# Kernel optimization log

Hardware: AMD Instinct MI355X
Metric: run time of the kernel (lower is better)

Reference implementation:

```python
import jax, jax.numpy as jnp
import numpy as np

N = 50000      # nodes
E = 800000     # edges (avg degree 16)
DN = 128       # in_node_feats (== out_feats)
DE = 64        # in_edge_feats
DO = 128       # out_feats


def setup_inputs() -> dict:
    key = jax.random.key(0)
    k1, k2, k3, k4, k5 = jax.random.split(key, 5)
    node_feats = jax.random.normal(k1, (N, DN), dtype=jnp.float32)
    edge_feats = jax.random.normal(k2, (E, DE), dtype=jnp.float32)
    src = jax.random.randint(k3, (E,), 0, N, dtype=jnp.int64) if jax.config.jax_enable_x64 else jax.random.randint(k3, (E,), 0, N).astype(jnp.int32)
    dst = jax.random.randint(k4, (E,), 0, N).astype(src.dtype)
    # nn.Linear(2*DN+DE, DO): weight [DO, 2*DN+DE], bias [DO]
    W = jax.random.normal(k5, (DO, 2 * DN + DE), dtype=jnp.float32) * 0.05
    b = jnp.zeros((DO,), dtype=jnp.float32)
    return {"node_feats": node_feats, "edge_feats": edge_feats, "W": W, "b": b, "src": src, "dst": dst}


def reference(node_feats, edge_feats, W, b, src, dst):
    # message: linear(cat([h_src, h_dst, e_f])) per edge -> [E, DO]
    msg_in = jnp.concatenate([node_feats[src], node_feats[dst], edge_feats], axis=1)  # [E, 2*DN+DE]
    mail = msg_in @ W.T + b                                                           # [E, DO]
    # scatter-mean at destination nodes (DGL mailbox mean)
    sums = jax.ops.segment_sum(mail, dst, num_segments=N)                             # [N, DO]
    deg = jax.ops.segment_sum(jnp.ones((mail.shape[0],), mail.dtype), dst, num_segments=N)  # [N]
    mean = sums / jnp.maximum(deg, 1.0)[:, None]
    # nodes with no incoming messages keep their original h (DGL update_all semantics)
    h = jnp.where(deg[:, None] > 0, mean, node_feats)
    # activation (relu); dropout is identity in eval / p=0
    return jax.nn.relu(h)
```

## Files before the change

### kernel.cpp

```cpp
#include <hip/hip_runtime.h>

#define DN 128
#define DE 64
#define DO 128
#define DIN 320
#define LDX 72
#define PAD 64

typedef short bf16x8 __attribute__((ext_vector_type(8)));
typedef float f32x4 __attribute__((ext_vector_type(4)));
typedef unsigned long long u64;

__device__ inline unsigned short f2bf(float f) {
    unsigned u = __builtin_bit_cast(unsigned, f);
    u = (u + 0x7fffu + ((u >> 16) & 1u)) >> 16;
    return (unsigned short)u;
}
__device__ inline unsigned pk2(float a, float b) {
    return (unsigned)f2bf(a) | ((unsigned)f2bf(b) << 16);
}
__device__ inline float bf2f(unsigned short h) {
    unsigned u = ((unsigned)h) << 16;
    return __builtin_bit_cast(float, u);
}
__device__ inline unsigned f2fp8(float f) {
    unsigned u = __builtin_bit_cast(unsigned, f * 0x1p-120f);
    unsigned s = (u >> 24) & 0x80u;
    u &= 0x7fffffffu;
    unsigned r = (u + 0x7ffffu + ((u >> 20) & 1u)) >> 20;
    if (r > 0x7eu) r = 0x7eu;
    return s | r;
}
__device__ inline float fp8_acc(unsigned b, float acc) {
    unsigned u = ((b & 0x80u) << 24) | ((b & 0x7fu) << 20);
    return fmaf(__builtin_bit_cast(float, u), 0x1p120f, acc);
}

__global__ __launch_bounds__(256) void convert_kernel(
    const float* __restrict__ W, const float* __restrict__ nf,
    unsigned short* __restrict__ Wbf, unsigned short* __restrict__ nfbf,
    unsigned char* __restrict__ nf8, int* __restrict__ cursor,
    int nW4, int n4tot, int N)
{
    int i = blockIdx.x * 256 + threadIdx.x;
    if (i < N) cursor[i] = 0;
    if (i >= n4tot) return;
    if (i < nW4) {
        const float4 v = *(const float4*)&W[(size_t)i * 4];
        u64 val = (u64)pk2(v.x, v.y) | ((u64)pk2(v.z, v.w) << 32);
        *(u64*)&Wbf[(size_t)i * 4] = val;
    } else {
        int j = i - nW4;
        const float4 v = *(const float4*)&nf[(size_t)j * 4];
        u64 val = (u64)pk2(v.x, v.y) | ((u64)pk2(v.z, v.w) << 32);
        *(u64*)&nfbf[(size_t)j * 4] = val;
        unsigned p8 = f2fp8(v.x) | (f2fp8(v.y) << 8) |
                      (f2fp8(v.z) << 16) | (f2fp8(v.w) << 24);
        *(unsigned*)&nf8[(size_t)j * 4] = p8;
    }
}

__global__ __launch_bounds__(256) void fill_kernel(
    const int* __restrict__ dst, const int* __restrict__ src,
    int* __restrict__ cursor, u64* __restrict__ es, int E)
{
    int e = blockIdx.x * 256 + threadIdx.x;
    if (e >= E) return;
    int d = dst[e];
    int s = src[e];
    int pos = atomicAdd(&cursor[d], 1);
    if (pos < PAD)
        es[(size_t)d * PAD + pos] = (u64)(unsigned)e | ((u64)(unsigned)s << 32);
}

__global__ __launch_bounds__(256) void gather_kernel(
    const unsigned char* __restrict__ nf8, const float* __restrict__ ef,
    const u64* __restrict__ es, const int* __restrict__ cursor,
    unsigned short* __restrict__ agg_src_bf,
    unsigned short* __restrict__ agg_edge_bf, int N)
{
    const int wave = threadIdx.x >> 6;
    const int lane = threadIdx.x & 63;
    const int v = blockIdx.x * 4 + wave;
    if (v >= N) return;

    const int cnt = min(cursor[v], PAD);

    const int g = lane >> 4;
    const int q = lane & 15;

    float accN[8];
#pragma unroll
    for (int j = 0; j < 8; ++j) accN[j] = 0.f;
    f32x4 accE = {0.f, 0.f, 0.f, 0.f};

    int e_l = 0, s_l = 0;
    if (lane < cnt) {
        u64 p = __builtin_nontemporal_load(&es[(size_t)v * PAD + lane]);
        e_l = (int)(unsigned)(p & 0xffffffffu);
        s_l = (int)(unsigned)(p >> 32);
    }
    for (int i = 0; i < cnt; i += 16) {
        const int s0 = __shfl(s_l, i + g, 64);
        const int s1 = __shfl(s_l, i + 4 + g, 64);
        const int s2 = __shfl(s_l, i + 8 + g, 64);
        const int s3 = __shfl(s_l, i + 12 + g, 64);
        const int e0 = __shfl(e_l, i + g, 64);
        const int e1 = __shfl(e_l, i + 4 + g, 64);
        const int e2 = __shfl(e_l, i + 8 + g, 64);
        const int e3 = __shfl(e_l, i + 12 + g, 64);
        u64 n0 = *(const u64*)&nf8[(size_t)s0 * DN + q * 8];
        u64 n1 = *(const u64*)&nf8[(size_t)s1 * DN + q * 8];
        u64 n2 = *(const u64*)&nf8[(size_t)s2 * DN + q * 8];
        u64 n3 = *(const u64*)&nf8[(size_t)s3 * DN + q * 8];
        f32x4 f0 = __builtin_nontemporal_load((const f32x4*)&ef[(size_t)e0 * DE + q * 4]);
        f32x4 f1 = __builtin_nontemporal_load((const f32x4*)&ef[(size_t)e1 * DE + q * 4]);
        f32x4 f2 = __builtin_nontemporal_load((const f32x4*)&ef[(size_t)e2 * DE + q * 4]);
        f32x4 f3 = __builtin_nontemporal_load((const f32x4*)&ef[(size_t)e3 * DE + q * 4]);
        if (i + g < cnt) {
#pragma unroll
            for (int j = 0; j < 8; ++j) accN[j] = fp8_acc((unsigned)(n0 >> (j * 8)) & 0xffu, accN[j]);
            accE += f0;
        }
        if (i + 4 + g < cnt) {
#pragma unroll
            for (int j = 0; j < 8; ++j) accN[j] = fp8_acc((unsigned)(n1 >> (j * 8)) & 0xffu, accN[j]);
            accE += f1;
        }
        if (i + 8 + g < cnt) {
#pragma unroll
            for (int j = 0; j < 8; ++j) accN[j] = fp8_acc((unsigned)(n2 >> (j * 8)) & 0xffu, accN[j]);
            accE += f2;
        }
        if (i + 12 + g < cnt) {
#pragma unroll
            for (int j = 0; j < 8; ++j) accN[j] = fp8_acc((unsigned)(n3 >> (j * 8)) & 0xffu, accN[j]);
            accE += f3;
        }
    }

#pragma unroll
    for (int j = 0; j < 8; ++j) {
        accN[j] += __shfl_xor(accN[j], 16, 64);
        accN[j] += __shfl_xor(accN[j], 32, 64);
    }
#pragma unroll
    for (int j = 0; j < 4; ++j) {
        accE[j] += __shfl_xor(accE[j], 16, 64);
        accE[j] += __shfl_xor(accE[j], 32, 64);
    }

    const float inv = (cnt > 0) ? (1.0f / (float)cnt) : 0.0f;
    if (g == 0) {
        uint4 val;
        val.x = pk2(accN[0] * inv, accN[1] * inv);
        val.y = pk2(accN[2] * inv, accN[3] * inv);
        val.z = pk2(accN[4] * inv, accN[5] * inv);
        val.w = pk2(accN[6] * inv, accN[7] * inv);
        *(uint4*)&agg_src_bf[(size_t)v * DN + q * 8] = val;
    } else if (g == 1) {
        u64 val = (u64)pk2(accE[0] * inv, accE[1] * inv) |
                  ((u64)pk2(accE[2] * inv, accE[3] * inv) << 32);
        *(u64*)&agg_edge_bf[(size_t)v * DE + q * 4] = val;
    }
}

__global__ __launch_bounds__(256) void finalize_kernel(
    const float* __restrict__ nf, const unsigned short* __restrict__ nfbf,
    const unsigned short* __restrict__ Wbf, const float* __restrict__ b,
    const unsigned short* __restrict__ agg_src_bf,
    const unsigned short* __restrict__ agg_edge_bf,
    const int* __restrict__ cursor, float* __restrict__ out, int N)
{
    __shared__ unsigned short Ws[DO * LDX];
    __shared__ unsigned short Xs[64 * LDX];
    __shared__ float bs[DO];
    __shared__ int degs[64];

    const int tid = threadIdx.x;
    const int lane = tid & 63;
    const int w = tid >> 6;
    const int node0 = blockIdx.x * 64;

    if (tid < DO) bs[tid] = b[tid];
    if (tid < 64) {
        int v = node0 + tid;
        degs[tid] = (v < N) ? cursor[v] : 0;
    }

    f32x4 acc[8];
#pragma unroll
    for (int r = 0; r < 8; ++r) acc[r] = (f32x4){0.f, 0.f, 0.f, 0.f};

    for (int c = 0; c < 5; ++c) {
        const int k0 = c * 64;
        __syncthreads();
#pragma unroll
        for (int it = 0; it < 8; ++it) {
            int i4 = tid + it * 256;
            int o = i4 >> 4;
            int kk = (i4 & 15) * 4;
            *(u64*)&Ws[o * LDX + kk] = *(const u64*)&Wbf[o * DIN + k0 + kk];
        }
#pragma unroll
        for (int it = 0; it < 4; ++it) {
            int i4 = tid + it * 256;
            int n = i4 >> 4;
            int kk = (i4 & 15) * 4;
            int v = node0 + n;
            u64 val = 0;
            if (v < N) {
                if (c < 2) {
                    val = *(const u64*)&agg_src_bf[(size_t)v * DN + k0 + kk];
                } else if (c < 4) {
                    val = *(const u64*)&nfbf[(size_t)v * DN + (c - 2) * 64 + kk];
                } else {
                    val = *(const u64*)&agg_edge_bf[(size_t)v * DE + kk];
                }
            }
            *(u64*)&Xs[n * LDX + kk] = val;
        }
        __syncthreads();

        const int xrow = 16 * w + (lane & 15);
        const int kgrp = (lane >> 4) * 8;
#pragma unroll
        for (int t = 0; t < 2; ++t) {
            bf16x8 a = *(const bf16x8*)&Xs[xrow * LDX + t * 32 + kgrp];
#pragma unroll
            for (int r = 0; r < 8; ++r) {
                bf16x8 bw = *(const bf16x8*)&Ws[(16 * r + (lane & 15)) * LDX + t * 32 + kgrp];
                acc[r] = __builtin_amdgcn_mfma_f32_16x16x32_bf16(a, bw, acc[r], 0, 0, 0);
            }
        }
    }

    const int col = lane & 15;
#pragma unroll
    for (int r = 0; r < 8; ++r) {
        const int o = 16 * r + col;
        const float bo = bs[o];
#pragma unroll
        for (int reg = 0; reg < 4; ++reg) {
            const int n = 16 * w + (lane >> 4) * 4 + reg;
            const int v = node0 + n;
            if (v >= N) continue;
            float val = (degs[n] > 0) ? (acc[r][reg] + bo) : nf[(size_t)v * DN + o];
            __builtin_nontemporal_store(fmaxf(val, 0.0f), &out[(size_t)v * DO + o]);
        }
    }
}

extern "C" void kernel_launch(void* const* d_in, const int* in_sizes, int n_in,
                              void* d_out, int out_size, void* d_ws, size_t ws_size,
                              hipStream_t stream)
{
    const float* nf  = (const float*)d_in[0];
    const float* ef  = (const float*)d_in[1];
    const float* W   = (const float*)d_in[2];
    const float* b   = (const float*)d_in[3];
    const int*   src = (const int*)d_in[4];
    const int*   dst = (const int*)d_in[5];
    float* out = (float*)d_out;

    const int N = in_sizes[0] / DN;
    const int E = in_sizes[4];

    char* p = (char*)d_ws;
    int* cursor = (int*)p;  p += (size_t)N * 4;
    p = (char*)(((uintptr_t)p + 15) & ~(uintptr_t)15);
    u64* es     = (u64*)p;  p += (size_t)N * PAD * 8;
    unsigned short* agg_src_bf  = (unsigned short*)p;  p += (size_t)N * DN * 2;
    unsigned short* agg_edge_bf = (unsigned short*)p;  p += (size_t)N * DE * 2;
    unsigned short* nfbf        = (unsigned short*)p;  p += (size_t)N * DN * 2;
    unsigned char*  nf8         = (unsigned char*)p;   p += (size_t)N * DN;
    unsigned short* Wbf         = (unsigned short*)p;

    const int nW4 = DO * DIN / 4;
    const int n4tot = nW4 + N * DN / 4;
    convert_kernel<<<(n4tot + 255) / 256, 256, 0, stream>>>(
        W, nf, Wbf, nfbf, nf8, cursor, nW4, n4tot, N);

    const int eb = (E + 255) / 256;
    fill_kernel<<<eb, 256, 0, stream>>>(dst, src, cursor, es, E);

    const int gb = (N + 3) / 4;
    gather_kernel<<<gb, 256, 0, stream>>>(nf8, ef, es, cursor,
                                          agg_src_bf, agg_edge_bf, N);

    const int nb = (N + 63) / 64;
    finalize_kernel<<<nb, 256, 0, stream>>>(nf, nfbf, Wbf, b, agg_src_bf,
                                            agg_edge_bf, cursor, out, N);
}
```

Before: 133.7 us.

## Merge convert and fill kernels; gather two nodes per wave

The dtype conversion and the CSR bucket fill now run in one kernel over a combined index range, and the cursor is zeroed with a memset instead of inside the convert kernel. This trades one kernel launch for a memset. The gather kernel now handles two destination nodes per wave, issuing twice as many independent loads per iteration to hide memory latency. The cost is more registers, which can lower occupancy, and iterating to the larger of the two degrees.

Result: slower. 167.1 us (+25.0%).

```diff
diff --git a/kernel.cpp b/kernel.cpp
--- a/kernel.cpp
+++ b/kernel.cpp
@@ -18,10 +18,6 @@
 }
 __device__ inline unsigned pk2(float a, float b) {
     return (unsigned)f2bf(a) | ((unsigned)f2bf(b) << 16);
-}
-__device__ inline float bf2f(unsigned short h) {
-    unsigned u = ((unsigned)h) << 16;
-    return __builtin_bit_cast(float, u);
 }
 __device__ inline unsigned f2fp8(float f) {
     unsigned u = __builtin_bit_cast(unsigned, f * 0x1p-120f);
@@ -36,41 +32,39 @@
     return fmaf(__builtin_bit_cast(float, u), 0x1p120f, acc);
 }
 
-__global__ __launch_bounds__(256) void convert_kernel(
+__global__ __launch_bounds__(256) void prep_kernel(
     const float* __restrict__ W, const float* __restrict__ nf,
     unsigned short* __restrict__ Wbf, unsigned short* __restrict__ nfbf,
-    unsigned char* __restrict__ nf8, int* __restrict__ cursor,
-    int nW4, int n4tot, int N)
+    unsigned char* __restrict__ nf8,
+    const int* __restrict__ dst, const int* __restrict__ src,
+    int* __restrict__ cursor, u64* __restrict__ es,
+    int nW4, int n4tot, int E)
 {
-    int i = blockIdx.x * 256 + threadIdx.x;
-    if (i < N) cursor[i] = 0;
-    if (i >= n4tot) return;
-    if (i < nW4) {
-        const float4 v = *(const float4*)&W[(size_t)i * 4];
-        u64 val = (u64)pk2(v.x, v.y) | ((u64)pk2(v.z, v.w) << 32);
-        *(u64*)&Wbf[(size_t)i * 4] = val;
+    int gid = blockIdx.x * 256 + threadIdx.x;
+    if (gid < n4tot) {
+        if (gid < nW4) {
+            const float4 v = *(const float4*)&W[(size_t)gid * 4];
+            u64 val = (u64)pk2(v.x, v.y) | ((u64)pk2(v.z, v.w) << 32);
+            *(u64*)&Wbf[(size_t)gid * 4] = val;
+        } else {
+            int j = gid - nW4;
+            const float4 v = *(const float4*)&nf[(size_t)j * 4];
+            u64 val = (u64)pk2(v.x, v.y) | ((u64)pk2(v.z, v.w) << 32);
+            *(u64*)&nfbf[(size_t)j * 4] = val;
+            unsigned p8 = f2fp8(v.x) | (f2fp8(v.y) << 8) |
+                          (f2fp8(v.z) << 16) | (f2fp8(v.w) << 24);
+            *(unsigned*)&nf8[(size_t)j * 4] = p8;
+        }
     } else {
-        int j = i - nW4;
-        const float4 v = *(const float4*)&nf[(size_t)j * 4];
-        u64 val = (u64)pk2(v.x, v.y) | ((u64)pk2(v.z, v.w) << 32);
-        *(u64*)&nfbf[(size_t)j * 4] = val;
-        unsigned p8 = f2fp8(v.x) | (f2fp8(v.y) << 8) |
-                      (f2fp8(v.z) << 16) | (f2fp8(v.w) << 24);
-        *(unsigned*)&nf8[(size_t)j * 4] = p8;
-    }
-}
-
-__global__ __launch_bounds__(256) void fill_kernel(
-    const int* __restrict__ dst, const int* __restrict__ src,
-    int* __restrict__ cursor, u64* __restrict__ es, int E)
-{
-    int e = blockIdx.x * 256 + threadIdx.x;
-    if (e >= E) return;
-    int d = dst[e];
-    int s = src[e];
-    int pos = atomicAdd(&cursor[d], 1);
-    if (pos < PAD)
-        es[(size_t)d * PAD + pos] = (u64)(unsigned)e | ((u64)(unsigned)s << 32);
+        int e = gid - n4tot;
+        if (e < E) {
+            int d = dst[e];
+            int s = src[e];
+            int pos = atomicAdd(&cursor[d], 1);
+            if (pos < PAD)
+                es[(size_t)d * PAD + pos] = (u64)(unsigned)e | ((u64)(unsigned)s << 32);
+        }
+    }
 }
 
 __global__ __launch_bounds__(256) void gather_kernel(
@@ -81,87 +75,150 @@
 {
     const int wave = threadIdx.x >> 6;
     const int lane = threadIdx.x & 63;
-    const int v = blockIdx.x * 4 + wave;
-    if (v >= N) return;
-
-    const int cnt = min(cursor[v], PAD);
+    const int v0 = blockIdx.x * 8 + wave * 2;
+    const int v1 = v0 + 1;
+    if (v0 >= N) return;
 
     const int g = lane >> 4;
     const int q = lane & 15;
 
-    float accN[8];
-#pragma unroll
-    for (int j = 0; j < 8; ++j) accN[j] = 0.f;
-    f32x4 accE = {0.f, 0.f, 0.f, 0.f};
-
-    int e_l = 0, s_l = 0;
-    if (lane < cnt) {
-        u64 p = __builtin_nontemporal_load(&es[(size_t)v * PAD + lane]);
-        e_l = (int)(unsigned)(p & 0xffffffffu);
-        s_l = (int)(unsigned)(p >> 32);
-    }
-    for (int i = 0; i < cnt; i += 16) {
-        const int s0 = __shfl(s_l, i + g, 64);
-        const int s1 = __shfl(s_l, i + 4 + g, 64);
-        const int s2 = __shfl(s_l, i + 8 + g, 64);
-        const int s3 = __shfl(s_l, i + 12 + g, 64);
-        const int e0 = __shfl(e_l, i + g, 64);
-        const int e1 = __shfl(e_l, i + 4 + g, 64);
-        const int e2 = __shfl(e_l, i + 8 + g, 64);
-        const int e3 = __shfl(e_l, i + 12 + g, 64);
-        u64 n0 = *(const u64*)&nf8[(size_t)s0 * DN + q * 8];
-        u64 n1 = *(const u64*)&nf8[(size_t)s1 * DN + q * 8];
-        u64 n2 = *(const u64*)&nf8[(size_t)s2 * DN + q * 8];
-        u64 n3 = *(const u64*)&nf8[(size_t)s3 * DN + q * 8];
-        f32x4 f0 = __builtin_nontemporal_load((const f32x4*)&ef[(size_t)e0 * DE + q * 4]);
-        f32x4 f1 = __builtin_nontemporal_load((const f32x4*)&ef[(size_t)e1 * DE + q * 4]);
-        f32x4 f2 = __builtin_nontemporal_load((const f32x4*)&ef[(size_t)e2 * DE + q * 4]);
-        f32x4 f3 = __builtin_nontemporal_load((const f32x4*)&ef[(size_t)e3 * DE + q * 4]);
-        if (i + g < cnt) {
-#pragma unroll
-            for (int j = 0; j < 8; ++j) accN[j] = fp8_acc((unsigned)(n0 >> (j * 8)) & 0xffu, accN[j]);
-            accE += f0;
-        }
-        if (i + 4 + g < cnt) {
-#pragma unroll
-            for (int j = 0; j < 8; ++j) accN[j] = fp8_acc((unsigned)(n1 >> (j * 8)) & 0xffu, accN[j]);
-            accE += f1;
-        }
-        if (i + 8 + g < cnt) {
-#pragma unroll
-            for (int j = 0; j < 8; ++j) accN[j] = fp8_acc((unsigned)(n2 >> (j * 8)) & 0xffu, accN[j]);
-            accE += f2;
-        }
-        if (i + 12 + g < cnt) {
-#pragma unroll
-            for (int j = 0; j < 8; ++j) accN[j] = fp8_acc((unsigned)(n3 >> (j * 8)) & 0xffu, accN[j]);
-            accE += f3;
+    const int cnt0 = min(cursor[v0], PAD);
+    const int cnt1 = (v1 < N) ? min(cursor[v1], PAD) : 0;
+
+    float accNA[8], accNB[8];
+#pragma unroll
+    for (int j = 0; j < 8; ++j) { accNA[j] = 0.f; accNB[j] = 0.f; }
+    f32x4 accEA = {0.f, 0.f, 0.f, 0.f};
+    f32x4 accEB = {0.f, 0.f, 0.f, 0.f};
+
+    int eA = 0, sA = 0, eB = 0, sB = 0;
+    if (lane < cnt0) {
+        u64 p = __builtin_nontemporal_load(&es[(size_t)v0 * PAD + lane]);
+        eA = (int)(unsigned)(p & 0xffffffffu);
+        sA = (int)(unsigned)(p >> 32);
+    }
+    if (lane < cnt1) {
+        u64 p = __builtin_nontemporal_load(&es[(size_t)v1 * PAD + lane]);
+        eB = (int)(unsigned)(p & 0xffffffffu);
+        sB = (int)(unsigned)(p >> 32);
+    }
+
+    const int cmax = max(cnt0, cnt1);
+    for (int i = 0; i < cmax; i += 16) {
+        const int sA0 = __shfl(sA, i + g, 64);
+        const int sA1 = __shfl(sA, i + 4 + g, 64);
+        const int sA2 = __shfl(sA, i + 8 + g, 64);
+        const int sA3 = __shfl(sA, i + 12 + g, 64);
+        const int eA0 = __shfl(eA, i + g, 64);
+        const int eA1 = __shfl(eA, i + 4 + g, 64);
+        const int eA2 = __shfl(eA, i + 8 + g, 64);
+        const int eA3 = __shfl(eA, i + 12 + g, 64);
+        const int sB0 = __shfl(sB, i + g, 64);
+        const int sB1 = __shfl(sB, i + 4 + g, 64);
+        const int sB2 = __shfl(sB, i + 8 + g, 64);
+        const int sB3 = __shfl(sB, i + 12 + g, 64);
+        const int eB0 = __shfl(eB, i + g, 64);
+        const int eB1 = __shfl(eB, i + 4 + g, 64);
+        const int eB2 = __shfl(eB, i + 8 + g, 64);
+        const int eB3 = __shfl(eB, i + 12 + g, 64);
+        u64 nA0 = *(const u64*)&nf8[(size_t)sA0 * DN + q * 8];
+        u64 nA1 = *(const u64*)&nf8[(size_t)sA1 * DN + q * 8];
+        u64 nA2 = *(const u64*)&nf8[(size_t)sA2 * DN + q * 8];
+        u64 nA3 = *(const u64*)&nf8[(size_t)sA3 * DN + q * 8];
+        u64 nB0 = *(const u64*)&nf8[(size_t)sB0 * DN + q * 8];
+        u64 nB1 = *(const u64*)&nf8[(size_t)sB1 * DN + q * 8];
+        u64 nB2 = *(const u64*)&nf8[(size_t)sB2 * DN + q * 8];
+        u64 nB3 = *(const u64*)&nf8[(size_t)sB3 * DN + q * 8];
+        f32x4 fA0 = __builtin_nontemporal_load((const f32x4*)&ef[(size_t)eA0 * DE + q * 4]);
+        f32x4 fA1 = __builtin_nontemporal_load((const f32x4*)&ef[(size_t)eA1 * DE + q * 4]);
+        f32x4 fA2 = __builtin_nontemporal_load((const f32x4*)&ef[(size_t)eA2 * DE + q * 4]);
+        f32x4 fA3 = __builtin_nontemporal_load((const f32x4*)&ef[(size_t)eA3 * DE + q * 4]);
+        f32x4 fB0 = __builtin_nontemporal_load((const f32x4*)&ef[(size_t)eB0 * DE + q * 4]);
+        f32x4 fB1 = __builtin_nontemporal_load((const f32x4*)&ef[(size_t)eB1 * DE + q * 4]);
+        f32x4 fB2 = __builtin_nontemporal_load((const f32x4*)&ef[(size_t)eB2 * DE + q * 4]);
+        f32x4 fB3 = __builtin_nontemporal_load((const f32x4*)&ef[(size_t)eB3 * DE + q * 4]);
+        if (i + g < cnt0) {
+#pragma unroll
+            for (int j = 0; j < 8; ++j) accNA[j] = fp8_acc((unsigned)(nA0 >> (j * 8)) & 0xffu, accNA[j]);
+            accEA += fA0;
+        }
+        if (i + 4 + g < cnt0) {
+#pragma unroll
+            for (int j = 0; j < 8; ++j) accNA[j] = fp8_acc((unsigned)(nA1 >> (j * 8)) & 0xffu, accNA[j]);
+            accEA += fA1;
+        }
+        if (i + 8 + g < cnt0) {
+#pragma unroll
+            for (int j = 0; j < 8; ++j) accNA[j] = fp8_acc((unsigned)(nA2 >> (j * 8)) & 0xffu, accNA[j]);
+            accEA += fA2;
+        }
+        if (i + 12 + g < cnt0) {
+#pragma unroll
+            for (int j = 0; j < 8; ++j) accNA[j] = fp8_acc((unsigned)(nA3 >> (j * 8)) & 0xffu, accNA[j]);
+            accEA += fA3;
+        }
+        if (i + g < cnt1) {
+#pragma unroll
+            for (int j = 0; j < 8; ++j) accNB[j] = fp8_acc((unsigned)(nB0 >> (j * 8)) & 0xffu, accNB[j]);
+            accEB += fB0;
+        }
+        if (i + 4 + g < cnt1) {
+#pragma unroll
+            for (int j = 0; j < 8; ++j) accNB[j] = fp8_acc((unsigned)(nB1 >> (j * 8)) & 0xffu, accNB[j]);
+            accEB += fB1;
+        }
+        if (i + 8 + g < cnt1) {
+#pragma unroll
+            for (int j = 0; j < 8; ++j) accNB[j] = fp8_acc((unsigned)(nB2 >> (j * 8)) & 0xffu, accNB[j]);
+            accEB += fB2;
+        }
+        if (i + 12 + g < cnt1) {
+#pragma unroll
+            for (int j = 0; j < 8; ++j) accNB[j] = fp8_acc((unsigned)(nB3 >> (j * 8)) & 0xffu, accNB[j]);
+            accEB += fB3;
         }
     }
 
 #pragma unroll
     for (int j = 0; j < 8; ++j) {
-        accN[j] += __shfl_xor(accN[j], 16, 64);
-        accN[j] += __shfl_xor(accN[j], 32, 64);
+        accNA[j] += __shfl_xor(accNA[j], 16, 64);
+        accNA[j] += __shfl_xor(accNA[j], 32, 64);
+        accNB[j] += __shfl_xor(accNB[j], 16, 64);
+        accNB[j] += __shfl_xor(accNB[j], 32, 64);
     }
 #pragma unroll
     for (int j = 0; j < 4; ++j) {
-        accE[j] += __shfl_xor(accE[j], 16, 64);
-        accE[j] += __shfl_xor(accE[j], 32, 64);
-    }
-
-    const float inv = (cnt > 0) ? (1.0f / (float)cnt) : 0.0f;
+        accEA[j] += __shfl_xor(accEA[j], 16, 64);
+        accEA[j] += __shfl_xor(accEA[j], 32, 64);
+        accEB[j] += __shfl_xor(accEB[j], 16, 64);
+        accEB[j] += __shfl_xor(accEB[j], 32, 64);
+    }
+
+    const float invA = (cnt0 > 0) ? (1.0f / (float)cnt0) : 0.0f;
+    const float invB = (cnt1 > 0) ? (1.0f / (float)cnt1) : 0.0f;
     if (g == 0) {
         uint4 val;
-        val.x = pk2(accN[0] * inv, accN[1] * inv);
-        val.y = pk2(accN[2] * inv, accN[3] * inv);
-        val.z = pk2(accN[4] * inv, accN[5] * inv);
-        val.w = pk2(accN[6] * inv, accN[7] * inv);
-        *(uint4*)&agg_src_bf[(size_t)v * DN + q * 8] = val;
+        val.x = pk2(accNA[0] * invA, accNA[1] * invA);
+        val.y = pk2(accNA[2] * invA, accNA[3] * invA);
+        val.z = pk2(accNA[4] * invA, accNA[5] * invA);
+        val.w = pk2(accNA[6] * invA, accNA[7] * invA);
+        *(uint4*)&agg_src_bf[(size_t)v0 * DN + q * 8] = val;
+        if (v1 < N) {
+            val.x = pk2(accNB[0] * invB, accNB[1] * invB);
+            val.y = pk2(accNB[2] * invB, accNB[3] * invB);
+            val.z = pk2(accNB[4] * invB, accNB[5] * invB);
+            val.w = pk2(accNB[6] * invB, accNB[7] * invB);
+            *(uint4*)&agg_src_bf[(size_t)v1 * DN + q * 8] = val;
+        }
     } else if (g == 1) {
-        u64 val = (u64)pk2(accE[0] * inv, accE[1] * inv) |
-                  ((u64)pk2(accE[2] * inv, accE[3] * inv) << 32);
-        *(u64*)&agg_edge_bf[(size_t)v * DE + q * 4] = val;
+        u64 val = (u64)pk2(accEA[0] * invA, accEA[1] * invA) |
+                  ((u64)pk2(accEA[2] * invA, accEA[3] * invA) << 32);
+        *(u64*)&agg_edge_bf[(size_t)v0 * DE + q * 4] = val;
+        if (v1 < N) {
+            val = (u64)pk2(accEB[0] * invB, accEB[1] * invB) |
+                  ((u64)pk2(accEB[2] * invB, accEB[3] * invB) << 32);
+            *(u64*)&agg_edge_bf[(size_t)v1 * DE + q * 4] = val;
+        }
     }
 }
 
@@ -276,15 +333,15 @@
     unsigned char*  nf8         = (unsigned char*)p;   p += (size_t)N * DN;
     unsigned short* Wbf         = (unsigned short*)p;
 
+    (void)hipMemsetAsync(cursor, 0, (size_t)N * sizeof(int), stream);
+
     const int nW4 = DO * DIN / 4;
     const int n4tot = nW4 + N * DN / 4;
-    convert_kernel<<<(n4tot + 255) / 256, 256, 0, stream>>>(
-        W, nf, Wbf, nfbf, nf8, cursor, nW4, n4tot, N);
-
-    const int eb = (E + 255) / 256;
-    fill_kernel<<<eb, 256, 0, stream>>>(dst, src, cursor, es, E);
-
-    const int gb = (N + 3) / 4;
+    const int prep_threads = n4tot + E;
+    prep_kernel<<<(prep_threads + 255) / 256, 256, 0, stream>>>(
+        W, nf, Wbf, nfbf, nf8, dst, src, cursor, es, nW4, n4tot, E);
+
+    const int gb = (N + 7) / 8;
     gather_kernel<<<gb, 256, 0, stream>>>(nf8, ef, es, cursor,
                                           agg_src_bf, agg_edge_bf, N);
 
```
